# Performance work log

Hardware: AMD Instinct MI355X
Metric: run time of the kernel (lower is better)

Reference implementation:

```python
import jax, jax.numpy as jnp
import numpy as np

EPS_LN = 1e-5
EPS_NORM = 1e-12
TEMP = 0.07

def _layernorm(x, g, b):
    m = jnp.mean(x, axis=-1, keepdims=True)
    v = jnp.var(x, axis=-1, keepdims=True)
    return (x - m) * jax.lax.rsqrt(v + EPS_LN) * g + b

def _l2norm(x):
    n = jnp.linalg.norm(x, axis=-1, keepdims=True)
    return x / jnp.maximum(n, EPS_NORM)

def setup_inputs() -> dict:
    key = jax.random.key(0)
    ks = jax.random.split(key, 8)
    B, N, Df, Dp, K = 64, 4096, 384, 256, 8
    H = W = 64
    def w(k, shp, scale):
        return jax.random.normal(k, shp, jnp.float32) * scale
    return {
        "patch_features": jax.random.normal(ks[0], (B, N, Df), jnp.float32),
        "H": H, "W": W,
        "W_proj": w(ks[1], (Df, Dp), 0.03), "b_proj": jnp.zeros((Dp,), jnp.float32),
        "g1": jnp.ones((Dp,), jnp.float32), "beta1": jnp.zeros((Dp,), jnp.float32),
        "prototypes": w(ks[2], (K, Dp), 0.02),
        "g2": jnp.ones((Dp,), jnp.float32), "beta2": jnp.zeros((Dp,), jnp.float32),
        "W_r1": w(ks[3], (Dp, 2 * Dp), 0.03), "b_r1": jnp.zeros((2 * Dp,), jnp.float32),
        "W_r2": w(ks[4], (2 * Dp, Dp), 0.03), "b_r2": jnp.zeros((Dp,), jnp.float32),
        "W_s1": w(ks[5], (Dp, 64), 0.05), "b_s1": jnp.zeros((64,), jnp.float32),
        "W_s2": w(ks[6], (64, 1), 0.05), "b_s2": jnp.zeros((1,), jnp.float32),
    }

def reference(patch_features, H, W, W_proj, b_proj, g1, beta1, prototypes,
              g2, beta2, W_r1, b_r1, W_r2, b_r2, W_s1, b_s1, W_s2, b_s2):
    gelu = lambda x: jax.nn.gelu(x, approximate=False)  # torch exact GELU
    # feat_proj: Linear -> LayerNorm -> GELU   [B,N,Dp]
    feat = gelu(_layernorm(patch_features @ W_proj + b_proj, g1, beta1))
    feat_norm = _l2norm(feat)
    proto_norm = _l2norm(prototypes)
    sim = jnp.einsum('bnd,kd->bnk', feat_norm, proto_norm) / TEMP
    assign = jax.nn.softmax(sim, axis=-1)            # [B,N,K]
    mass = jnp.clip(assign.sum(axis=1), 1e-6, None)[:, :, None]  # [B,K,1]
    part_feat = jnp.einsum('bnk,bnd->bkd', assign, feat) / mass  # [B,K,Dp]
    # refine MLP: LN -> Linear(2Dp) -> GELU -> Linear(Dp), residual add
    h = _layernorm(part_feat, g2, beta2)
    part_feat = part_feat + (gelu(h @ W_r1 + b_r1) @ W_r2 + b_r2)
    # normalized grid coordinates [N,2] = (x, y)
    gy = jnp.arange(H, dtype=jnp.float32) / max(H - 1, 1)
    gx = jnp.arange(W, dtype=jnp.float32) / max(W - 1, 1)
    grid_y, grid_x = jnp.meshgrid(gy, gx, indexing='ij')
    coords = jnp.stack([grid_x.reshape(-1), grid_y.reshape(-1)], axis=-1)
    part_pos = jnp.einsum('bnk,nc->bkc', assign, coords) / mass  # [B,K,2]
    salience = jax.nn.sigmoid(gelu(part_feat @ W_s1 + b_s1) @ W_s2 + b_s2)[..., 0]
    return (part_feat, part_pos, assign, salience, feat)
```

## Files before the change

kernel.cpp:

```cpp
#include <hip/hip_runtime.h>
#include <hip/hip_bf16.h>
#include <stdint.h>
#include <stddef.h>

#define DF 384
#define DP 256
#define NPROT 8
#define NPB 4096
#define KSTEPS 12

typedef __attribute__((ext_vector_type(8))) short bf16x8;
typedef __attribute__((ext_vector_type(4))) short bf16x4;
typedef __attribute__((ext_vector_type(4))) float f32x4;

typedef const __attribute__((address_space(1))) unsigned char as1_u8;
typedef __attribute__((address_space(3))) unsigned char as3_u8;

static __device__ __forceinline__ short f2bf(float f) {
  __hip_bfloat16 h(f);
  return *reinterpret_cast<short*>(&h);
}
static __device__ __forceinline__ float gelu_f(float x) {
  float x3 = x * x * x;
  float t = __expf(1.5957691216057308f * fmaf(0.044715f, x3, x));
  return x - x / (t + 1.0f);
}

static __device__ __forceinline__ f32x4 mfma16x16x16_bf16(bf16x4 a, bf16x4 b, f32x4 c) {
#if __has_builtin(__builtin_amdgcn_mfma_f32_16x16x16bf16_1k)
  return __builtin_amdgcn_mfma_f32_16x16x16bf16_1k(a, b, c, 0, 0, 0);
#else
  asm volatile("v_mfma_f32_16x16x16_bf16 %0, %1, %2, %0" : "+v"(c) : "v"(a), "v"(b));
  return c;
#endif
}

__global__ __launch_bounds__(256) void k_setup(const float* __restrict__ W,
                                               unsigned short* __restrict__ wT,
                                               const float* __restrict__ P,
                                               float* __restrict__ PN,
                                               unsigned short* __restrict__ pb) {
  if (blockIdx.x < 384) {
    int e = blockIdx.x * 256 + threadIdx.x;
    int c = e / DF;
    int k = e - c * DF;
    wT[e] = (unsigned short)f2bf(W[k * DP + c]);
  } else {
    __shared__ float s_red[4];
    __shared__ float s_pn[NPROT][DP];
    const int tid = threadIdx.x;
    const int lane = tid & 63, wave = tid >> 6;
    for (int r = 0; r < NPROT; r++) {
      float x = P[r * DP + tid];
      float q = x * x;
      #pragma unroll
      for (int d = 1; d < 64; d <<= 1) q += __shfl_xor(q, d);
      if (lane == 0) s_red[wave] = q;
      __syncthreads();
      float ss = s_red[0] + s_red[1] + s_red[2] + s_red[3];
      float v = x / fmaxf(sqrtf(ss), 1e-12f);
      PN[r * DP + tid] = v;
      s_pn[r][tid] = v;
      __syncthreads();
    }
    for (int i = tid; i < 512; i += 256) {
      int step = i >> 6, l = i & 63;
      int k = l & 15, g = l >> 4;
      bf16x8 v;
      #pragma unroll
      for (int j = 0; j < 8; j++) {
        int d = step * 32 + g * 8 + j;
        v[j] = (k < NPROT) ? f2bf(s_pn[k][d]) : (short)0;
      }
      *(bf16x8*)(pb + (size_t)i * 8) = v;
    }
  }
}

__global__ __launch_bounds__(256, 3) void k_fused(
    const float* __restrict__ patch,
    const float* __restrict__ bias,
    const float* __restrict__ g1,
    const float* __restrict__ beta1,
    const unsigned short* __restrict__ wT,
    const unsigned short* __restrict__ pb,
    float* __restrict__ out_feat,
    float* __restrict__ out_assign,
    float* __restrict__ part_partial,
    float* __restrict__ mp_partial,
    float* __restrict__ acc_part,
    float* __restrict__ acc_mass,
    float* __restrict__ acc_pos,
    int use_part) {
  __shared__ __align__(16) unsigned char Bbuf[33792];
  __shared__ __align__(16) unsigned short s_pb[512 * 8];
  __shared__ float s_bias[DP], s_g1[DP], s_b1[DP];
  __shared__ float s_mp[4][3][NPROT];

  const int tid  = threadIdx.x;
  const int lane = tid & 63;
  const int wave = tid >> 6;
  const int mrow = lane & 15;
  const int kgrp = lane >> 4;

  const long long row0 = (long long)blockIdx.x * 64;
  const int b  = (int)(row0 >> 12);
  const int n0 = (int)(row0 & 4095);

  s_bias[tid] = bias[tid];
  s_g1[tid]   = g1[tid];
  s_b1[tid]   = beta1[tid];
  *(bf16x8*)(s_pb + (size_t)tid * 8)         = *(const bf16x8*)(pb + (size_t)tid * 8);
  *(bf16x8*)(s_pb + (size_t)(256 + tid) * 8) = *(const bf16x8*)(pb + (size_t)(256 + tid) * 8);

  #define STAGE(kt_, q_)                                                        \
    {                                                                           \
      _Pragma("unroll")                                                         \
      for (int i = 0; i < 4; i++) {                                             \
        int e   = i * 256 + tid;                                                \
        int col = e >> 2;                                                       \
        int t4  = e & 3;                                                        \
        int sub = t4 ^ ((col >> 1) & 3);                                        \
        const unsigned short* src = wT + col * DF + (kt_) * 32 + sub * 8;       \
        int lofs = __builtin_amdgcn_readfirstlane(                              \
            (q_) * 16384 + (i * 256 + wave * 64) * 16);                         \
        __builtin_amdgcn_global_load_lds((as1_u8*)(const void*)src,             \
                                         (as3_u8*)(void*)(Bbuf + lofs), 16, 0, 0); \
      }                                                                         \
    }

  STAGE(0, 0);
  const float* arow = patch + (size_t)(row0 + wave * 16 + mrow) * DF + kgrp * 8;
  bf16x8 afrag[KSTEPS];
  #pragma unroll
  for (int kt = 0; kt < KSTEPS; kt++) {
    float4 x0 = *(const float4*)(arow + kt * 32);
    float4 x1 = *(const float4*)(arow + kt * 32 + 4);
    bf16x8 a;
    a[0] = f2bf(x0.x); a[1] = f2bf(x0.y); a[2] = f2bf(x0.z); a[3] = f2bf(x0.w);
    a[4] = f2bf(x1.x); a[5] = f2bf(x1.y); a[6] = f2bf(x1.z); a[7] = f2bf(x1.w);
    afrag[kt] = a;
  }

  f32x4 acc[16];
  #pragma unroll
  for (int f = 0; f < 16; f++) acc[f] = (f32x4){0.f, 0.f, 0.f, 0.f};

  __syncthreads();

  const int lane_swz = mrow * 64 + (kgrp ^ ((mrow >> 1) & 3)) * 16;

  #pragma unroll
  for (int kt = 0; kt < KSTEPS; kt++) {
    if (kt + 1 < KSTEPS) STAGE(kt + 1, (kt + 1) & 1);
    const unsigned char* bbase = Bbuf + (kt & 1) * 16384 + lane_swz;
    bf16x8 a = afrag[kt];
    #pragma unroll
    for (int f = 0; f < 16; f++) {
      bf16x8 bf = *(const bf16x8*)(bbase + f * 1024);
      acc[f] = __builtin_amdgcn_mfma_f32_16x16x32_bf16(a, bf, acc[f], 0, 0, 0);
    }
    asm volatile("s_waitcnt vmcnt(0) lgkmcnt(0)" ::: "memory");
    __builtin_amdgcn_s_barrier();
    __builtin_amdgcn_sched_barrier(0);
  }
  #undef STAGE

  #pragma unroll
  for (int f = 0; f < 16; f++) {
    const float bb = s_bias[f * 16 + mrow];
    #pragma unroll
    for (int r = 0; r < 4; r++) acc[f][r] += bb;
  }
  #pragma unroll
  for (int r = 0; r < 4; r++) {
    float s = 0.f, q = 0.f;
    #pragma unroll
    for (int f = 0; f < 16; f++) { float x = acc[f][r]; s += x; q += x * x; }
    #pragma unroll
    for (int d = 1; d < 16; d <<= 1) { s += __shfl_xor(s, d); q += __shfl_xor(q, d); }
    const float mean = s * (1.f / 256.f);
    const float var  = q * (1.f / 256.f) - mean * mean;
    const float rstd = rsqrtf(var + 1e-5f);
    #pragma unroll
    for (int f = 0; f < 16; f++) {
      const int col = f * 16 + mrow;
      float y = (acc[f][r] - mean) * rstd * s_g1[col] + s_b1[col];
      acc[f][r] = gelu_f(y);
    }
  }

  float ssn[4];
  #pragma unroll
  for (int r = 0; r < 4; r++) {
    float q2 = 0.f;
    #pragma unroll
    for (int f = 0; f < 16; f++) q2 += acc[f][r] * acc[f][r];
    #pragma unroll
    for (int d = 1; d < 16; d <<= 1) q2 += __shfl_xor(q2, d);
    ssn[r] = q2;
  }

  f32x4 cdot = (f32x4){0.f, 0.f, 0.f, 0.f};
  {
    float* s_tr = (float*)Bbuf;
    const int rr = lane >> 5;
    const int cc = (lane & 31) * 4;
    float* fb = out_feat + (size_t)(row0 + wave * 16) * DP;
    const int aoff = (wave * 16 + mrow) * 132 + kgrp * 8;
    #pragma unroll
    for (int p = 0; p < 2; p++) {
      #pragma unroll
      for (int fl = 0; fl < 8; fl++) {
        const int f = 8 * p + fl;
        #pragma unroll
        for (int r = 0; r < 4; r++)
          s_tr[(wave * 16 + kgrp * 4 + r) * 132 + fl * 16 + mrow] = acc[f][r];
      }
      #pragma unroll
      for (int i = 0; i < 8; i++) {
        const int row = i * 2 + rr;
        f32x4 v = *(const f32x4*)&s_tr[(wave * 16 + row) * 132 + cc];
        *(f32x4*)&fb[(size_t)row * DP + p * 128 + cc] = v;
      }
      #pragma unroll
      for (int s = 0; s < 4; s++) {
        float4 y0 = *(const float4*)&s_tr[aoff + s * 32];
        float4 y1 = *(const float4*)&s_tr[aoff + s * 32 + 4];
        bf16x8 a;
        a[0] = f2bf(y0.x); a[1] = f2bf(y0.y); a[2] = f2bf(y0.z); a[3] = f2bf(y0.w);
        a[4] = f2bf(y1.x); a[5] = f2bf(y1.y); a[6] = f2bf(y1.z); a[7] = f2bf(y1.w);
        bf16x8 pf = *(const bf16x8*)(s_pb + (size_t)((p * 4 + s) * 64 + lane) * 8);
        cdot = __builtin_amdgcn_mfma_f32_16x16x32_bf16(a, pf, cdot, 0, 0, 0);
      }
    }
  }

  float asg[4];
  #pragma unroll
  for (int r = 0; r < 4; r++) {
    const float nrm = fmaxf(sqrtf(ssn[r]), 1e-12f);
    float lg = (mrow < NPROT) ? (cdot[r] / nrm) * (1.f / 0.07f) : -1e30f;
    float mx = lg;
    #pragma unroll
    for (int d = 1; d < 16; d <<= 1) mx = fmaxf(mx, __shfl_xor(mx, d));
    float e = __expf(lg - mx);
    float se = e;
    #pragma unroll
    for (int d = 1; d < 16; d <<= 1) se += __shfl_xor(se, d);
    asg[r] = e / se;
  }

  float pm = 0.f, px = 0.f, py = 0.f;
  #pragma unroll
  for (int r = 0; r < 4; r++) {
    const int n = n0 + wave * 16 + kgrp * 4 + r;
    if (mrow < NPROT)
      out_assign[((size_t)b * NPB + n) * NPROT + mrow] = asg[r];
    const float cx = (float)(n & 63) * (1.f / 63.f);
    const float cy = (float)(n >> 6) * (1.f / 63.f);
    pm += asg[r]; px += asg[r] * cx; py += asg[r] * cy;
  }
  pm += __shfl_xor(pm, 16); pm += __shfl_xor(pm, 32);
  px += __shfl_xor(px, 16); px += __shfl_xor(px, 32);
  py += __shfl_xor(py, 16); py += __shfl_xor(py, 32);
  if (lane < NPROT) {
    s_mp[wave][0][lane] = pm;
    s_mp[wave][1][lane] = px;
    s_mp[wave][2][lane] = py;
  }

  __syncthreads();

  {
    float* s_partw = (float*)Bbuf;
    bf16x4 a4;
    #pragma unroll
    for (int j = 0; j < 4; j++) a4[j] = f2bf(asg[j]);
    #pragma unroll
    for (int f = 0; f < 16; f++) {
      bf16x4 b4;
      #pragma unroll
      for (int j = 0; j < 4; j++) b4[j] = f2bf(acc[f][j]);
      f32x4 c = mfma16x16x16_bf16(a4, b4, (f32x4){0.f, 0.f, 0.f, 0.f});
      if (kgrp < 2) {
        #pragma unroll
        for (int r = 0; r < 4; r++)
          s_partw[((wave * 8 + kgrp * 4 + r)) * 256 + f * 16 + mrow] = c[r];
      }
    }
  }
  __syncthreads();

  {
    const float* s_partw = (const float*)Bbuf;
    float pr[NPROT];
    #pragma unroll
    for (int k = 0; k < NPROT; k++)
      pr[k] = s_partw[(0 * 8 + k) * 256 + tid] + s_partw[(1 * 8 + k) * 256 + tid] +
              s_partw[(2 * 8 + k) * 256 + tid] + s_partw[(3 * 8 + k) * 256 + tid];

    if (use_part) {
      float* pp = part_partial + (size_t)blockIdx.x * 2048;
      #pragma unroll
      for (int k = 0; k < NPROT; k++) pp[k * 256 + tid] = pr[k];
      if (tid < 24) {
        const int v = tid >> 3, k = tid & 7;
        float s = s_mp[0][v][k] + s_mp[1][v][k] + s_mp[2][v][k] + s_mp[3][v][k];
        mp_partial[(size_t)blockIdx.x * 32 + v * 8 + k] = s;
      }
    } else {
      float* gp = acc_part + (size_t)b * (NPROT * DP);
      #pragma unroll
      for (int k = 0; k < NPROT; k++) atomicAdd(&gp[k * 256 + tid], pr[k]);
      if (tid < 24) {
        const int v = tid >> 3, k = tid & 7;
        float s = s_mp[0][v][k] + s_mp[1][v][k] + s_mp[2][v][k] + s_mp[3][v][k];
        if (v == 0) atomicAdd(&acc_mass[b * NPROT + k], s);
        else        atomicAdd(&acc_pos[(b * NPROT + k) * 2 + (v - 1)], s);
      }
    }
  }
}

__global__ __launch_bounds__(256) void k_reduce(const float* __restrict__ pp,
                                                float* __restrict__ acc_part) {
  const int b = blockIdx.x >> 3;
  const int j = blockIdx.x & 7;
  const int col = j * 256 + threadIdx.x;
  const float* base = pp + (size_t)b * 64 * 2048 + col;
  float a0 = 0.f, a1 = 0.f, a2 = 0.f, a3 = 0.f;
  #pragma unroll
  for (int p = 0; p < 64; p += 4) {
    a0 += base[(size_t)p * 2048];
    a1 += base[(size_t)(p + 1) * 2048];
    a2 += base[(size_t)(p + 2) * 2048];
    a3 += base[(size_t)(p + 3) * 2048];
  }
  acc_part[(size_t)b * 2048 + col] = (a0 + a1) + (a2 + a3);
}

__global__ __launch_bounds__(256) void k_final(
    const float* __restrict__ mp_partial,
    const float* __restrict__ acc_part, const float* __restrict__ acc_mass,
    const float* __restrict__ acc_pos,
    const float* __restrict__ g2, const float* __restrict__ beta2,
    const float* __restrict__ W_r1, const float* __restrict__ b_r1,
    const float* __restrict__ W_r2, const float* __restrict__ b_r2,
    const float* __restrict__ W_s1, const float* __restrict__ b_s1,
    const float* __restrict__ W_s2, const float* __restrict__ b_s2,
    float* __restrict__ out_pf, float* __restrict__ out_pos, float* __restrict__ out_sal,
    int use_part) {
  __shared__ float s_pf[8 * DP];
  __shared__ float s_h[8 * DP];
  __shared__ float s_t[8 * 512];
  __shared__ float s_pff[8 * DP];
  __shared__ float s_s1v[8 * 64];
  __shared__ float s_m[8];
  __shared__ float s_red[8];
  const int b = blockIdx.x;
  const int tid = threadIdx.x;
  const int lane = tid & 63, wave = tid >> 6;

  if (use_part) {
    if (tid < 8) {
      float m = 0.f, x = 0.f, y = 0.f;
      for (int j = 0; j < 64; j++) {
        const float* q = mp_partial + ((size_t)b * 64 + j) * 32;
        m += q[tid]; x += q[8 + tid]; y += q[16 + tid];
      }
      m = fmaxf(m, 1e-6f);
      s_m[tid] = m;
      out_pos[b * 16 + tid * 2 + 0] = x / m;
      out_pos[b * 16 + tid * 2 + 1] = y / m;
    }
  } else {
    if (tid < 8) s_m[tid] = fmaxf(acc_mass[b * 8 + tid], 1e-6f);
    if (tid >= 64 && tid < 80) {
      int t = tid - 64;
      out_pos[b * 16 + t] = acc_pos[b * 16 + t] / fmaxf(acc_mass[b * 8 + (t >> 1)], 1e-6f);
    }
  }
  __syncthreads();
  #pragma unroll
  for (int i = 0; i < 8; i++) {
    int idx = i * 256 + tid;
    s_pf[idx] = acc_part[(size_t)b * 2048 + idx] / s_m[i];
  }
  __syncthreads();

  for (int r = 0; r < 8; r++) {
    float x = s_pf[r * DP + tid];
    float s = x, q = x * x;
    #pragma unroll
    for (int d = 1; d < 64; d <<= 1) { s += __shfl_xor(s, d); q += __shfl_xor(q, d); }
    if (lane == 0) { s_red[wave] = s; s_red[4 + wave] = q; }
    __syncthreads();
    float ts = s_red[0] + s_red[1] + s_red[2] + s_red[3];
    float tq = s_red[4] + s_red[5] + s_red[6] + s_red[7];
    float mean = ts * (1.f / 256.f);
    float var  = tq * (1.f / 256.f) - mean * mean;
    s_h[r * DP + tid] = (x - mean) * rsqrtf(var + 1e-5f) * g2[tid] + beta2[tid];
    __syncthreads();
  }

  #pragma unroll
  for (int i = 0; i < 2; i++) {
    const int o = i * 256 + tid;
    float a[8];
    #pragma unroll
    for (int r = 0; r < 8; r++) a[r] = 0.f;
    #pragma unroll 8
    for (int c = 0; c < DP; c++) {
      const float w = W_r1[c * 512 + o];
      #pragma unroll
      for (int r = 0; r < 8; r++) a[r] += s_h[r * DP + c] * w;
    }
    const float bb = b_r1[o];
    #pragma unroll
    for (int r = 0; r < 8; r++) s_t[r * 512 + o] = gelu_f(a[r] + bb);
  }
  __syncthreads();

  {
    const int o = tid;
    float a[8];
    #pragma unroll
    for (int r = 0; r < 8; r++) a[r] = 0.f;
    #pragma unroll 8
    for (int c = 0; c < 512; c++) {
      const float w = W_r2[c * DP + o];
      #pragma unroll
      for (int r = 0; r < 8; r++) a[r] += s_t[r * 512 + c] * w;
    }
    const float bb = b_r2[o];
    #pragma unroll
    for (int r = 0; r < 8; r++) {
      float v = s_pf[r * DP + o] + a[r] + bb;
      s_pff[r * DP + o] = v;
      out_pf[(size_t)b * 2048 + r * DP + o] = v;
    }
  }
  __syncthreads();

  if (tid < 64) {
    const int o = tid;
    float a[8];
    #pragma unroll
    for (int r = 0; r < 8; r++) a[r] = 0.f;
    #pragma unroll 8
    for (int c = 0; c < DP; c++) {
      const float w = W_s1[c * 64 + o];
      #pragma unroll
      for (int r = 0; r < 8; r++) a[r] += s_pff[r * DP + c] * w;
    }
    const float bb = b_s1[o];
    #pragma unroll
    for (int r = 0; r < 8; r++) s_s1v[r * 64 + o] = gelu_f(a[r] + bb);
  }
  __syncthreads();

  if (tid < 8) {
    float a = 0.f;
    for (int c = 0; c < 64; c++) a += s_s1v[tid * 64 + c] * W_s2[c];
    a += b_s2[0];
    out_sal[b * 8 + tid] = 1.f / (1.f + __expf(-a));
  }
}

extern "C" void kernel_launch(void* const* d_in, const int* in_sizes, int n_in,
                              void* d_out, int out_size, void* d_ws, size_t ws_size,
                              hipStream_t stream) {
  (void)in_sizes; (void)n_in; (void)out_size;
  const float* patch  = (const float*)d_in[0];
  const float* W_proj = (const float*)d_in[3];
  const float* b_proj = (const float*)d_in[4];
  const float* g1     = (const float*)d_in[5];
  const float* beta1  = (const float*)d_in[6];
  const float* proto  = (const float*)d_in[7];
  const float* g2     = (const float*)d_in[8];
  const float* beta2  = (const float*)d_in[9];
  const float* W_r1   = (const float*)d_in[10];
  const float* b_r1   = (const float*)d_in[11];
  const float* W_r2   = (const float*)d_in[12];
  const float* b_r2   = (const float*)d_in[13];
  const float* W_s1   = (const float*)d_in[14];
  const float* b_s1   = (const float*)d_in[15];
  const float* W_s2   = (const float*)d_in[16];
  const float* b_s2   = (const float*)d_in[17];

  float* out = (float*)d_out;
  float* out_pf     = out;
  float* out_pos    = out + 131072;
  float* out_assign = out + 132096;
  float* out_sal    = out + 2229248;
  float* out_feat   = out + 2229760;

  char* ws = (char*)d_ws;
  unsigned short* wT  = (unsigned short*)ws;
  float* protoN       = (float*)(ws + 196608);
  unsigned short* pbf = (unsigned short*)(ws + 204800);
  float* acc_part     = (float*)(ws + 262144);
  float* acc_mass     = (float*)(ws + 786432);
  float* acc_pos      = (float*)(ws + 788480);
  float* part_partial = (float*)(ws + 1048576);
  float* mp_partial   = (float*)(ws + 1048576 + 33554432);

  const size_t need_part = 1048576ull + 33554432ull + 524288ull;
  const int use_part = (ws_size >= need_part) ? 1 : 0;

  if (!use_part) hipMemsetAsync(ws + 262144, 0, 530432, stream);
  k_setup<<<385, 256, 0, stream>>>(W_proj, wT, proto, protoN, pbf);
  k_fused<<<4096, 256, 0, stream>>>(patch, b_proj, g1, beta1, wT, pbf,
                                    out_feat, out_assign,
                                    part_partial, mp_partial,
                                    acc_part, acc_mass, acc_pos, use_part);
  if (use_part) k_reduce<<<512, 256, 0, stream>>>(part_partial, acc_part);
  k_final<<<64, 256, 0, stream>>>(mp_partial, acc_part, acc_mass, acc_pos,
                                  g2, beta2, W_r1, b_r1, W_r2, b_r2,
                                  W_s1, b_s1, W_s2, b_s2,
                                  out_pf, out_pos, out_sal, use_part);
}
```

Before: 329.8 us.

## Split fused kernel columns across two waves per row group with 512-thread blocks

Doubles the fused kernel's block to 512 threads. Each 16-row group is now handled by two waves, each computing half of the 256 output columns. Partial LayerNorm sums, L2 norms and prototype dot products are combined through shared memory with extra barriers, and only one wave per pair runs the softmax. The aim is to halve per-wave accumulator registers and raise occupancy, which should hide memory latency better. The cost is more shared-memory traffic and synchronisation, and duplicated A-fragment loads per wave pair.

```diff
diff --git a/kernel.cpp b/kernel.cpp
--- a/kernel.cpp
+++ b/kernel.cpp
@@ -77,7 +77,7 @@
   }
 }
 
-__global__ __launch_bounds__(256, 3) void k_fused(
+__global__ __launch_bounds__(512, 4) void k_fused(
     const float* __restrict__ patch,
     const float* __restrict__ bias,
     const float* __restrict__ g1,
@@ -92,14 +92,20 @@
     float* __restrict__ acc_mass,
     float* __restrict__ acc_pos,
     int use_part) {
-  __shared__ __align__(16) unsigned char Bbuf[33792];
+  __shared__ __align__(16) unsigned char Bbuf[35840];
   __shared__ __align__(16) unsigned short s_pb[512 * 8];
   __shared__ float s_bias[DP], s_g1[DP], s_b1[DP];
+  __shared__ float2 s_ln[2][64];
+  __shared__ float s_ss[2][64];
+  __shared__ __align__(16) float s_cd[8 * 64 * 4];
+  __shared__ float s_asg[64 * 8];
   __shared__ float s_mp[4][3][NPROT];
 
   const int tid  = threadIdx.x;
   const int lane = tid & 63;
   const int wave = tid >> 6;
+  const int rg   = wave >> 1;
+  const int ch   = wave & 1;
   const int mrow = lane & 15;
   const int kgrp = lane >> 4;
 
@@ -107,30 +113,29 @@
   const int b  = (int)(row0 >> 12);
   const int n0 = (int)(row0 & 4095);
 
-  s_bias[tid] = bias[tid];
-  s_g1[tid]   = g1[tid];
-  s_b1[tid]   = beta1[tid];
-  *(bf16x8*)(s_pb + (size_t)tid * 8)         = *(const bf16x8*)(pb + (size_t)tid * 8);
-  *(bf16x8*)(s_pb + (size_t)(256 + tid) * 8) = *(const bf16x8*)(pb + (size_t)(256 + tid) * 8);
+  if (tid < DP) {
+    s_bias[tid] = bias[tid];
+    s_g1[tid]   = g1[tid];
+    s_b1[tid]   = beta1[tid];
+  }
+  *(bf16x8*)(s_pb + (size_t)tid * 8) = *(const bf16x8*)(pb + (size_t)tid * 8);
+
+  const unsigned short* bsrc =
+      wT + (tid >> 2) * DF + ((tid & 3) ^ ((tid >> 3) & 3)) * 8;
+  const int lofs0 = __builtin_amdgcn_readfirstlane(wave * 1024);
 
   #define STAGE(kt_, q_)                                                        \
     {                                                                           \
       _Pragma("unroll")                                                         \
-      for (int i = 0; i < 4; i++) {                                             \
-        int e   = i * 256 + tid;                                                \
-        int col = e >> 2;                                                       \
-        int t4  = e & 3;                                                        \
-        int sub = t4 ^ ((col >> 1) & 3);                                        \
-        const unsigned short* src = wT + col * DF + (kt_) * 32 + sub * 8;       \
-        int lofs = __builtin_amdgcn_readfirstlane(                              \
-            (q_) * 16384 + (i * 256 + wave * 64) * 16);                         \
-        __builtin_amdgcn_global_load_lds((as1_u8*)(const void*)src,             \
-                                         (as3_u8*)(void*)(Bbuf + lofs), 16, 0, 0); \
+      for (int i = 0; i < 2; i++) {                                             \
+        __builtin_amdgcn_global_load_lds(                                       \
+            (as1_u8*)(const void*)(bsrc + i * 49152 + (kt_) * 32),              \
+            (as3_u8*)(void*)(Bbuf + (q_) * 16384 + i * 8192 + lofs0), 16, 0, 0);\
       }                                                                         \
     }
 
   STAGE(0, 0);
-  const float* arow = patch + (size_t)(row0 + wave * 16 + mrow) * DF + kgrp * 8;
+  const float* arow = patch + (size_t)(row0 + rg * 16 + mrow) * DF + kgrp * 8;
   bf16x8 afrag[KSTEPS];
   #pragma unroll
   for (int kt = 0; kt < KSTEPS; kt++) {
@@ -141,14 +146,12 @@
     a[4] = f2bf(x1.x); a[5] = f2bf(x1.y); a[6] = f2bf(x1.z); a[7] = f2bf(x1.w);
     afrag[kt] = a;
   }
-
-  f32x4 acc[16];
-  #pragma unroll
-  for (int f = 0; f < 16; f++) acc[f] = (f32x4){0.f, 0.f, 0.f, 0.f};
-
-  __syncthreads();
-
-  const int lane_swz = mrow * 64 + (kgrp ^ ((mrow >> 1) & 3)) * 16;
+  f32x4 acc[8];
+  #pragma unroll
+  for (int f = 0; f < 8; f++) acc[f] = (f32x4){0.f, 0.f, 0.f, 0.f};
+  __syncthreads();
+
+  const int lane_swz = ch * 8192 + mrow * 64 + (kgrp ^ ((mrow >> 1) & 3)) * 16;
 
   #pragma unroll
   for (int kt = 0; kt < KSTEPS; kt++) {
@@ -156,7 +159,7 @@
     const unsigned char* bbase = Bbuf + (kt & 1) * 16384 + lane_swz;
     bf16x8 a = afrag[kt];
     #pragma unroll
-    for (int f = 0; f < 16; f++) {
+    for (int f = 0; f < 8; f++) {
       bf16x8 bf = *(const bf16x8*)(bbase + f * 1024);
       acc[f] = __builtin_amdgcn_mfma_f32_16x16x32_bf16(a, bf, acc[f], 0, 0, 0);
     }
@@ -167,8 +170,8 @@
   #undef STAGE
 
   #pragma unroll
-  for (int f = 0; f < 16; f++) {
-    const float bb = s_bias[f * 16 + mrow];
+  for (int f = 0; f < 8; f++) {
+    const float bb = s_bias[ch * 128 + f * 16 + mrow];
     #pragma unroll
     for (int r = 0; r < 4; r++) acc[f][r] += bb;
   }
@@ -176,109 +179,124 @@
   for (int r = 0; r < 4; r++) {
     float s = 0.f, q = 0.f;
     #pragma unroll
-    for (int f = 0; f < 16; f++) { float x = acc[f][r]; s += x; q += x * x; }
+    for (int f = 0; f < 8; f++) { float x = acc[f][r]; s += x; q += x * x; }
     #pragma unroll
     for (int d = 1; d < 16; d <<= 1) { s += __shfl_xor(s, d); q += __shfl_xor(q, d); }
-    const float mean = s * (1.f / 256.f);
-    const float var  = q * (1.f / 256.f) - mean * mean;
+    if (mrow == 0) s_ln[ch][rg * 16 + kgrp * 4 + r] = make_float2(s, q);
+  }
+  __syncthreads();
+  #pragma unroll
+  for (int r = 0; r < 4; r++) {
+    const int grow = rg * 16 + kgrp * 4 + r;
+    float2 h0 = s_ln[0][grow], h1 = s_ln[1][grow];
+    const float mean = (h0.x + h1.x) * (1.f / 256.f);
+    const float var  = (h0.y + h1.y) * (1.f / 256.f) - mean * mean;
     const float rstd = rsqrtf(var + 1e-5f);
     #pragma unroll
-    for (int f = 0; f < 16; f++) {
-      const int col = f * 16 + mrow;
-      float y = (acc[f][r] - mean) * rstd * s_g1[col] + s_b1[col];
-      acc[f][r] = gelu_f(y);
-    }
-  }
-
-  float ssn[4];
+    for (int f = 0; f < 8; f++) {
+      const int col = ch * 128 + f * 16 + mrow;
+      acc[f][r] = gelu_f((acc[f][r] - mean) * rstd * s_g1[col] + s_b1[col]);
+    }
+  }
   #pragma unroll
   for (int r = 0; r < 4; r++) {
     float q2 = 0.f;
     #pragma unroll
-    for (int f = 0; f < 16; f++) q2 += acc[f][r] * acc[f][r];
+    for (int f = 0; f < 8; f++) q2 += acc[f][r] * acc[f][r];
     #pragma unroll
     for (int d = 1; d < 16; d <<= 1) q2 += __shfl_xor(q2, d);
-    ssn[r] = q2;
+    if (mrow == 0) s_ss[ch][rg * 16 + kgrp * 4 + r] = q2;
   }
 
   f32x4 cdot = (f32x4){0.f, 0.f, 0.f, 0.f};
   {
-    float* s_tr = (float*)Bbuf;
-    const int rr = lane >> 5;
-    const int cc = (lane & 31) * 4;
-    float* fb = out_feat + (size_t)(row0 + wave * 16) * DP;
-    const int aoff = (wave * 16 + mrow) * 132 + kgrp * 8;
+    float* s_trW = (float*)Bbuf + wave * 1088;
+    float* fb = out_feat + (size_t)(row0 + rg * 16) * DP + ch * 128;
+    const int aoff = mrow * 68 + kgrp * 8;
     #pragma unroll
     for (int p = 0; p < 2; p++) {
       #pragma unroll
-      for (int fl = 0; fl < 8; fl++) {
-        const int f = 8 * p + fl;
+      for (int fl = 0; fl < 4; fl++) {
+        const int f = p * 4 + fl;
         #pragma unroll
         for (int r = 0; r < 4; r++)
-          s_tr[(wave * 16 + kgrp * 4 + r) * 132 + fl * 16 + mrow] = acc[f][r];
-      }
-      #pragma unroll
-      for (int i = 0; i < 8; i++) {
-        const int row = i * 2 + rr;
-        f32x4 v = *(const f32x4*)&s_tr[(wave * 16 + row) * 132 + cc];
-        *(f32x4*)&fb[(size_t)row * DP + p * 128 + cc] = v;
-      }
-      #pragma unroll
-      for (int s = 0; s < 4; s++) {
-        float4 y0 = *(const float4*)&s_tr[aoff + s * 32];
-        float4 y1 = *(const float4*)&s_tr[aoff + s * 32 + 4];
+          s_trW[(kgrp * 4 + r) * 68 + fl * 16 + mrow] = acc[f][r];
+      }
+      #pragma unroll
+      for (int j = 0; j < 4; j++) {
+        const int idx = j * 64 + lane;
+        const int row = idx >> 4;
+        const int c4  = (idx & 15) * 4;
+        f32x4 v = *(const f32x4*)&s_trW[row * 68 + c4];
+        *(f32x4*)&fb[(size_t)row * DP + p * 64 + c4] = v;
+      }
+      #pragma unroll
+      for (int s = 0; s < 2; s++) {
+        float4 y0 = *(const float4*)&s_trW[aoff + s * 32];
+        float4 y1 = *(const float4*)&s_trW[aoff + s * 32 + 4];
         bf16x8 a;
         a[0] = f2bf(y0.x); a[1] = f2bf(y0.y); a[2] = f2bf(y0.z); a[3] = f2bf(y0.w);
         a[4] = f2bf(y1.x); a[5] = f2bf(y1.y); a[6] = f2bf(y1.z); a[7] = f2bf(y1.w);
-        bf16x8 pf = *(const bf16x8*)(s_pb + (size_t)((p * 4 + s) * 64 + lane) * 8);
+        const int step = ch * 4 + p * 2 + s;
+        bf16x8 pf = *(const bf16x8*)(s_pb + (size_t)(step * 64 + lane) * 8);
         cdot = __builtin_amdgcn_mfma_f32_16x16x32_bf16(a, pf, cdot, 0, 0, 0);
       }
     }
   }
-
-  float asg[4];
-  #pragma unroll
-  for (int r = 0; r < 4; r++) {
-    const float nrm = fmaxf(sqrtf(ssn[r]), 1e-12f);
-    float lg = (mrow < NPROT) ? (cdot[r] / nrm) * (1.f / 0.07f) : -1e30f;
-    float mx = lg;
-    #pragma unroll
-    for (int d = 1; d < 16; d <<= 1) mx = fmaxf(mx, __shfl_xor(mx, d));
-    float e = __expf(lg - mx);
-    float se = e;
-    #pragma unroll
-    for (int d = 1; d < 16; d <<= 1) se += __shfl_xor(se, d);
-    asg[r] = e / se;
-  }
-
-  float pm = 0.f, px = 0.f, py = 0.f;
-  #pragma unroll
-  for (int r = 0; r < 4; r++) {
-    const int n = n0 + wave * 16 + kgrp * 4 + r;
-    if (mrow < NPROT)
-      out_assign[((size_t)b * NPB + n) * NPROT + mrow] = asg[r];
-    const float cx = (float)(n & 63) * (1.f / 63.f);
-    const float cy = (float)(n >> 6) * (1.f / 63.f);
-    pm += asg[r]; px += asg[r] * cx; py += asg[r] * cy;
-  }
-  pm += __shfl_xor(pm, 16); pm += __shfl_xor(pm, 32);
-  px += __shfl_xor(px, 16); px += __shfl_xor(px, 32);
-  py += __shfl_xor(py, 16); py += __shfl_xor(py, 32);
-  if (lane < NPROT) {
-    s_mp[wave][0][lane] = pm;
-    s_mp[wave][1][lane] = px;
-    s_mp[wave][2][lane] = py;
-  }
-
+  *(f32x4*)&s_cd[(size_t)(wave * 64 + lane) * 4] = cdot;
+  __syncthreads();
+
+  if (ch == 0) {
+    f32x4 oth = *(const f32x4*)&s_cd[(size_t)((wave + 1) * 64 + lane) * 4];
+    float asg[4];
+    #pragma unroll
+    for (int r = 0; r < 4; r++) {
+      const int grow = rg * 16 + kgrp * 4 + r;
+      const float ssn = s_ss[0][grow] + s_ss[1][grow];
+      const float nrm = fmaxf(sqrtf(ssn), 1e-12f);
+      float lg = (mrow < NPROT) ? ((cdot[r] + oth[r]) / nrm) * (1.f / 0.07f) : -1e30f;
+      float mx = lg;
+      #pragma unroll
+      for (int d = 1; d < 16; d <<= 1) mx = fmaxf(mx, __shfl_xor(mx, d));
+      float e = __expf(lg - mx);
+      float se = e;
+      #pragma unroll
+      for (int d = 1; d < 16; d <<= 1) se += __shfl_xor(se, d);
+      asg[r] = e / se;
+    }
+    float pm = 0.f, px = 0.f, py = 0.f;
+    #pragma unroll
+    for (int r = 0; r < 4; r++) {
+      const int n = n0 + rg * 16 + kgrp * 4 + r;
+      if (mrow < NPROT) {
+        out_assign[((size_t)b * NPB + n) * NPROT + mrow] = asg[r];
+        s_asg[(rg * 16 + kgrp * 4 + r) * 8 + mrow] = asg[r];
+      }
+      const float cx = (float)(n & 63) * (1.f / 63.f);
+      const float cy = (float)(n >> 6) * (1.f / 63.f);
+      pm += asg[r]; px += asg[r] * cx; py += asg[r] * cy;
+    }
+    pm += __shfl_xor(pm, 16); pm += __shfl_xor(pm, 32);
+    px += __shfl_xor(px, 16); px += __shfl_xor(px, 32);
+    py += __shfl_xor(py, 16); py += __shfl_xor(py, 32);
+    if (lane < NPROT) {
+      s_mp[rg][0][lane] = pm;
+      s_mp[rg][1][lane] = px;
+      s_mp[rg][2][lane] = py;
+    }
+  }
   __syncthreads();
 
   {
     float* s_partw = (float*)Bbuf;
     bf16x4 a4;
     #pragma unroll
-    for (int j = 0; j < 4; j++) a4[j] = f2bf(asg[j]);
-    #pragma unroll
-    for (int f = 0; f < 16; f++) {
+    for (int j = 0; j < 4; j++) {
+      float v = (mrow < NPROT) ? s_asg[(rg * 16 + kgrp * 4 + j) * 8 + mrow] : 0.f;
+      a4[j] = f2bf(v);
+    }
+    #pragma unroll
+    for (int f = 0; f < 8; f++) {
       bf16x4 b4;
       #pragma unroll
       for (int j = 0; j < 4; j++) b4[j] = f2bf(acc[f][j]);
@@ -286,7 +304,7 @@
       if (kgrp < 2) {
         #pragma unroll
         for (int r = 0; r < 4; r++)
-          s_partw[((wave * 8 + kgrp * 4 + r)) * 256 + f * 16 + mrow] = c[r];
+          s_partw[(rg * 8 + kgrp * 4 + r) * 256 + ch * 128 + f * 16 + mrow] = c[r];
       }
     }
   }
@@ -294,16 +312,16 @@
 
   {
     const float* s_partw = (const float*)Bbuf;
-    float pr[NPROT];
-    #pragma unroll
-    for (int k = 0; k < NPROT; k++)
-      pr[k] = s_partw[(0 * 8 + k) * 256 + tid] + s_partw[(1 * 8 + k) * 256 + tid] +
-              s_partw[(2 * 8 + k) * 256 + tid] + s_partw[(3 * 8 + k) * 256 + tid];
-
     if (use_part) {
       float* pp = part_partial + (size_t)blockIdx.x * 2048;
       #pragma unroll
-      for (int k = 0; k < NPROT; k++) pp[k * 256 + tid] = pr[k];
+      for (int i = 0; i < 4; i++) {
+        const int idx = i * 512 + tid;
+        const int kp = idx >> 8, col = idx & 255;
+        float pr = s_partw[(0 * 8 + kp) * 256 + col] + s_partw[(1 * 8 + kp) * 256 + col] +
+                   s_partw[(2 * 8 + kp) * 256 + col] + s_partw[(3 * 8 + kp) * 256 + col];
+        pp[idx] = pr;
+      }
       if (tid < 24) {
         const int v = tid >> 3, k = tid & 7;
         float s = s_mp[0][v][k] + s_mp[1][v][k] + s_mp[2][v][k] + s_mp[3][v][k];
@@ -312,7 +330,13 @@
     } else {
       float* gp = acc_part + (size_t)b * (NPROT * DP);
       #pragma unroll
-      for (int k = 0; k < NPROT; k++) atomicAdd(&gp[k * 256 + tid], pr[k]);
+      for (int i = 0; i < 4; i++) {
+        const int idx = i * 512 + tid;
+        const int kp = idx >> 8, col = idx & 255;
+        float pr = s_partw[(0 * 8 + kp) * 256 + col] + s_partw[(1 * 8 + kp) * 256 + col] +
+                   s_partw[(2 * 8 + kp) * 256 + col] + s_partw[(3 * 8 + kp) * 256 + col];
+        atomicAdd(&gp[idx], pr);
+      }
       if (tid < 24) {
         const int v = tid >> 3, k = tid & 7;
         float s = s_mp[0][v][k] + s_mp[1][v][k] + s_mp[2][v][k] + s_mp[3][v][k];
@@ -511,7 +535,7 @@
 
   if (!use_part) hipMemsetAsync(ws + 262144, 0, 530432, stream);
   k_setup<<<385, 256, 0, stream>>>(W_proj, wT, proto, protoN, pbf);
-  k_fused<<<4096, 256, 0, stream>>>(patch, b_proj, g1, beta1, wT, pbf,
+  k_fused<<<4096, 512, 0, stream>>>(patch, b_proj, g1, beta1, wT, pbf,
                                     out_feat, out_assign,
                                     part_partial, mp_partial,
                                     acc_part, acc_mass, acc_pos, use_part);
```

Result: slower. 381.0 us (+15.5%).

## Widen k_final to 512 threads and split its serial reductions and matmuls

Applied to the files above, without the earlier changes.

Doubles the k_final block to 512 threads. It parallelises the mass/position partial reduction with shuffles and runs the per-row LayerNorm one wave per row, which removes the 8 serialized barrier rounds. The W_r1 matmul now gives each thread one output column. W_r2 and W_s1 are split across thread groups over the inner dimension, with partial sums combined through shared memory. This targets the latency of the small tail kernel that runs only 64 blocks, at the cost of more shared memory and extra barriers.

```diff
diff --git a/kernel.cpp b/kernel.cpp
--- a/kernel.cpp
+++ b/kernel.cpp
@@ -340,7 +340,7 @@
   acc_part[(size_t)b * 2048 + col] = (a0 + a1) + (a2 + a3);
 }
 
-__global__ __launch_bounds__(256) void k_final(
+__global__ __launch_bounds__(512) void k_final(
     const float* __restrict__ mp_partial,
     const float* __restrict__ acc_part, const float* __restrict__ acc_mass,
     const float* __restrict__ acc_pos,
@@ -357,22 +357,30 @@
   __shared__ float s_pff[8 * DP];
   __shared__ float s_s1v[8 * 64];
   __shared__ float s_m[8];
-  __shared__ float s_red[8];
+  __shared__ float s_mpred[24];
+  __shared__ float s_r2p[8 * DP];
+  __shared__ float s_s1p[8][8][64];
   const int b = blockIdx.x;
   const int tid = threadIdx.x;
   const int lane = tid & 63, wave = tid >> 6;
 
   if (use_part) {
-    if (tid < 8) {
-      float m = 0.f, x = 0.f, y = 0.f;
-      for (int j = 0; j < 64; j++) {
-        const float* q = mp_partial + ((size_t)b * 64 + j) * 32;
-        m += q[tid]; x += q[8 + tid]; y += q[16 + tid];
-      }
-      m = fmaxf(m, 1e-6f);
-      s_m[tid] = m;
-      out_pos[b * 16 + tid * 2 + 0] = x / m;
-      out_pos[b * 16 + tid * 2 + 1] = y / m;
+    if (tid < 384) {
+      const int vk = tid >> 4;
+      const int jt = tid & 15;
+      const int v = vk >> 3, k = vk & 7;
+      const float* q = mp_partial + ((size_t)b * 64 + jt * 4) * 32 + v * 8 + k;
+      float part = q[0] + q[32] + q[64] + q[96];
+      #pragma unroll
+      for (int d = 1; d < 16; d <<= 1) part += __shfl_xor(part, d);
+      if (jt == 0) s_mpred[vk] = part;
+    }
+    __syncthreads();
+    if (tid < 8) s_m[tid] = fmaxf(s_mpred[tid], 1e-6f);
+    __syncthreads();
+    if (tid < 16) {
+      const int k = tid >> 1, xy = tid & 1;
+      out_pos[b * 16 + tid] = s_mpred[(xy + 1) * 8 + k] / s_m[k];
     }
   } else {
     if (tid < 8) s_m[tid] = fmaxf(acc_mass[b * 8 + tid], 1e-6f);
@@ -380,33 +388,37 @@
       int t = tid - 64;
       out_pos[b * 16 + t] = acc_pos[b * 16 + t] / fmaxf(acc_mass[b * 8 + (t >> 1)], 1e-6f);
     }
-  }
-  __syncthreads();
-  #pragma unroll
-  for (int i = 0; i < 8; i++) {
-    int idx = i * 256 + tid;
-    s_pf[idx] = acc_part[(size_t)b * 2048 + idx] / s_m[i];
-  }
-  __syncthreads();
-
-  for (int r = 0; r < 8; r++) {
-    float x = s_pf[r * DP + tid];
-    float s = x, q = x * x;
+    __syncthreads();
+  }
+  __syncthreads();
+
+  #pragma unroll
+  for (int i = 0; i < 4; i++) {
+    const int idx = i * 512 + tid;
+    s_pf[idx] = acc_part[(size_t)b * 2048 + idx] / s_m[idx >> 8];
+  }
+  __syncthreads();
+
+  {
+    const int r = wave;
+    f32x4 x = *(const f32x4*)&s_pf[r * DP + lane * 4];
+    float s = x[0] + x[1] + x[2] + x[3];
+    float q = x[0] * x[0] + x[1] * x[1] + x[2] * x[2] + x[3] * x[3];
     #pragma unroll
     for (int d = 1; d < 64; d <<= 1) { s += __shfl_xor(s, d); q += __shfl_xor(q, d); }
-    if (lane == 0) { s_red[wave] = s; s_red[4 + wave] = q; }
-    __syncthreads();
-    float ts = s_red[0] + s_red[1] + s_red[2] + s_red[3];
-    float tq = s_red[4] + s_red[5] + s_red[6] + s_red[7];
-    float mean = ts * (1.f / 256.f);
-    float var  = tq * (1.f / 256.f) - mean * mean;
-    s_h[r * DP + tid] = (x - mean) * rsqrtf(var + 1e-5f) * g2[tid] + beta2[tid];
-    __syncthreads();
-  }
-
-  #pragma unroll
-  for (int i = 0; i < 2; i++) {
-    const int o = i * 256 + tid;
+    const float mean = s * (1.f / 256.f);
+    const float var  = q * (1.f / 256.f) - mean * mean;
+    const float rstd = rsqrtf(var + 1e-5f);
+    #pragma unroll
+    for (int j = 0; j < 4; j++) {
+      const int col = lane * 4 + j;
+      s_h[r * DP + col] = (x[j] - mean) * rstd * g2[col] + beta2[col];
+    }
+  }
+  __syncthreads();
+
+  {
+    const int o = tid;
     float a[8];
     #pragma unroll
     for (int r = 0; r < 8; r++) a[r] = 0.f;
@@ -423,40 +435,56 @@
   __syncthreads();
 
   {
-    const int o = tid;
+    const int g = tid >> 8, o = tid & 255;
     float a[8];
     #pragma unroll
     for (int r = 0; r < 8; r++) a[r] = 0.f;
     #pragma unroll 8
-    for (int c = 0; c < 512; c++) {
+    for (int cc = 0; cc < 256; cc++) {
+      const int c = g * 256 + cc;
       const float w = W_r2[c * DP + o];
       #pragma unroll
       for (int r = 0; r < 8; r++) a[r] += s_t[r * 512 + c] * w;
     }
-    const float bb = b_r2[o];
-    #pragma unroll
-    for (int r = 0; r < 8; r++) {
-      float v = s_pf[r * DP + o] + a[r] + bb;
-      s_pff[r * DP + o] = v;
-      out_pf[(size_t)b * 2048 + r * DP + o] = v;
-    }
-  }
-  __syncthreads();
-
-  if (tid < 64) {
-    const int o = tid;
+    if (g) {
+      #pragma unroll
+      for (int r = 0; r < 8; r++) s_r2p[r * DP + o] = a[r];
+    }
+    __syncthreads();
+    if (!g) {
+      const float bb = b_r2[o];
+      #pragma unroll
+      for (int r = 0; r < 8; r++) {
+        float v = s_pf[r * DP + o] + a[r] + s_r2p[r * DP + o] + bb;
+        s_pff[r * DP + o] = v;
+        out_pf[(size_t)b * 2048 + r * DP + o] = v;
+      }
+    }
+  }
+  __syncthreads();
+
+  {
+    const int o = tid & 63, g = tid >> 6;
     float a[8];
     #pragma unroll
     for (int r = 0; r < 8; r++) a[r] = 0.f;
     #pragma unroll 8
-    for (int c = 0; c < DP; c++) {
+    for (int cc = 0; cc < 32; cc++) {
+      const int c = g * 32 + cc;
       const float w = W_s1[c * 64 + o];
       #pragma unroll
       for (int r = 0; r < 8; r++) a[r] += s_pff[r * DP + c] * w;
     }
-    const float bb = b_s1[o];
-    #pragma unroll
-    for (int r = 0; r < 8; r++) s_s1v[r * 64 + o] = gelu_f(a[r] + bb);
+    #pragma unroll
+    for (int r = 0; r < 8; r++) s_s1p[g][r][o] = a[r];
+  }
+  __syncthreads();
+  {
+    const int r = tid >> 6, o = tid & 63;
+    float a = 0.f;
+    #pragma unroll
+    for (int g = 0; g < 8; g++) a += s_s1p[g][r][o];
+    s_s1v[r * 64 + o] = gelu_f(a + b_s1[o]);
   }
   __syncthreads();
 
@@ -516,7 +544,7 @@
                                     part_partial, mp_partial,
                                     acc_part, acc_mass, acc_pos, use_part);
   if (use_part) k_reduce<<<512, 256, 0, stream>>>(part_partial, acc_part);
-  k_final<<<64, 256, 0, stream>>>(mp_partial, acc_part, acc_mass, acc_pos,
+  k_final<<<64, 512, 0, stream>>>(mp_partial, acc_part, acc_mass, acc_pos,
                                   g2, beta2, W_r1, b_r1, W_r2, b_r2,
                                   W_s1, b_s1, W_s2, b_s2,
                                   out_pf, out_pos, out_sal, use_part);
```

Measured after the change: 282.0 us. 14.5% less time.
